# Kernel optimization log

Hardware: AMD Instinct MI355X
Metric: run time of the kernel (lower is better)

The kernel has to match this reference:

```python
import jax, jax.numpy as jnp
import numpy as np

M, K, N = 8192, 4096, 4096  # tokens, in_features, out_features
QMAX = 127.0


def setup_inputs() -> dict:
    key = jax.random.key(0)
    kx, kw, ks, kb = jax.random.split(key, 4)
    x = jax.random.normal(kx, (M, K), dtype=jnp.float32)
    # Build w_q / s_w the same way from_float would: per-output-channel symmetric quant
    w = jax.random.normal(kw, (N, K), dtype=jnp.float32) * 0.02
    s_w = (jnp.max(jnp.abs(w), axis=1, keepdims=True) / QMAX).astype(jnp.float32)  # [N,1]
    w_q = jnp.clip(jnp.round(w / s_w), -QMAX, QMAX).astype(jnp.int8)  # [N,K] int8
    bias = jax.random.normal(kb, (N,), dtype=jnp.float32) * 0.01
    return {"x": x, "w_q": w_q, "s_w": s_w, "bias": bias}


def reference(x, w_q, s_w, bias):
    # mode == 'W8A8_dynamic': per-tensor symmetric activation quant (zp = 0)
    s_x = jnp.max(jnp.abs(x)) / QMAX                       # scalar scale
    x_q = jnp.clip(jnp.round(x / s_x), -QMAX, QMAX)        # int8 values held in fp32
    # fake-dequant matmul: (x_q @ w_q^T) * (s_x * s_w^T) + bias
    y_int = x_q @ w_q.astype(jnp.float32).T                # [M, N]
    y = y_int * (s_x * s_w.astype(jnp.float32).T)          # broadcast [1,N]
    y = y + bias
    return y.astype(x.dtype)
```

## Files before the change

kernel.cpp:

```cpp
#include <hip/hip_runtime.h>
#include <stdint.h>

#define QMAXF 127.0f

constexpr int Mdim = 8192;
constexpr int Kdim = 4096;
constexpr int Ndim = 4096;
constexpr int PREP_BLOCKS = 2048;

using i32x4 = __attribute__((ext_vector_type(4))) int;

__device__ __forceinline__ void async_copy16(const void* g, void* l) {
    __builtin_amdgcn_global_load_lds(
        (const __attribute__((address_space(1))) void*)g,
        (__attribute__((address_space(3))) void*)l,
        16, 0, 0);
}

__global__ void prep_kernel(const float* __restrict__ x,
                            const int* __restrict__ w32,
                            float* __restrict__ blockmax,
                            int8_t* __restrict__ w8) {
    float m = 0.f;
    const float4* x4 = (const float4*)x;
    const int n4x = Mdim * Kdim / 4;
    for (int i = blockIdx.x * blockDim.x + threadIdx.x; i < n4x;
         i += gridDim.x * blockDim.x) {
        float4 v = x4[i];
        m = fmaxf(fmaxf(fabsf(v.x), fabsf(v.y)),
                  fmaxf(m, fmaxf(fabsf(v.z), fabsf(v.w))));
    }
#pragma unroll
    for (int off = 32; off > 0; off >>= 1)
        m = fmaxf(m, __shfl_down(m, off, 64));
    __shared__ float red[4];
    if ((threadIdx.x & 63) == 0) red[threadIdx.x >> 6] = m;
    __syncthreads();
    if (threadIdx.x == 0)
        blockmax[blockIdx.x] =
            fmaxf(fmaxf(red[0], red[1]), fmaxf(red[2], red[3]));

    const int4* in4 = (const int4*)w32;
    char4* out4 = (char4*)w8;
    const int n4w = Ndim * Kdim / 4;
    for (int i = blockIdx.x * blockDim.x + threadIdx.x; i < n4w;
         i += gridDim.x * blockDim.x) {
        int4 v = in4[i];
        char4 c;
        c.x = (signed char)v.x;
        c.y = (signed char)v.y;
        c.z = (signed char)v.z;
        c.w = (signed char)v.w;
        out4[i] = c;
    }
}

__global__ void finalize_kernel(const float* __restrict__ blockmax,
                                float* __restrict__ sx) {
    float m = 0.f;
    for (int i = threadIdx.x; i < PREP_BLOCKS; i += 256)
        m = fmaxf(m, blockmax[i]);
#pragma unroll
    for (int off = 32; off > 0; off >>= 1)
        m = fmaxf(m, __shfl_down(m, off, 64));
    __shared__ float red[4];
    if ((threadIdx.x & 63) == 0) red[threadIdx.x >> 6] = m;
    __syncthreads();
    if (threadIdx.x == 0)
        *sx = fmaxf(fmaxf(red[0], red[1]), fmaxf(red[2], red[3])) / QMAXF;
}

__global__ void quant_x_kernel(const float* __restrict__ x,
                               const float* __restrict__ sxp,
                               int8_t* __restrict__ xq, int n4) {
    const float s = *sxp;
    const float4* x4 = (const float4*)x;
    char4* q4 = (char4*)xq;
    for (int i = blockIdx.x * blockDim.x + threadIdx.x; i < n4;
         i += gridDim.x * blockDim.x) {
        float4 v = x4[i];
        char4 q;
        q.x = (signed char)(int)fminf(QMAXF, fmaxf(-QMAXF, rintf(v.x / s)));
        q.y = (signed char)(int)fminf(QMAXF, fmaxf(-QMAXF, rintf(v.y / s)));
        q.z = (signed char)(int)fminf(QMAXF, fmaxf(-QMAXF, rintf(v.z / s)));
        q.w = (signed char)(int)fminf(QMAXF, fmaxf(-QMAXF, rintf(v.w / s)));
        q4[i] = q;
    }
}

#define BM 256
#define BN 256
#define BKB 128
#define NKT (Kdim / BKB)

#define BAR() __builtin_amdgcn_s_barrier()
#define LGKM0()                                           \
    do {                                                  \
        asm volatile("s_waitcnt lgkmcnt(0)" ::: "memory");\
        __builtin_amdgcn_sched_barrier(0);                \
    } while (0)

__global__ __launch_bounds__(512, 2) void gemm_i8_kernel(
    const int8_t* __restrict__ Xq, const int8_t* __restrict__ Wq,
    const float* __restrict__ sxp, const float* __restrict__ s_w,
    const float* __restrict__ bias, float* __restrict__ Y) {
    __shared__ int8_t lds[131072];

    const int t = threadIdx.x;
    const int w = t >> 6;
    const int l = t & 63;
    const int lane15 = l & 15;
    const int lquad = l >> 4;
    const int swz7 = l & 7;

    const int flat = blockIdx.y * gridDim.x + blockIdx.x;
    const int swzb = (flat & 7) * 64 + (flat >> 3);
    const int bn = (swzb & 15) * BN;
    const int bm = (swzb >> 4) * BM;

    const int r0 = t >> 3;
    const int cOff = ((t & 7) ^ (r0 & 7)) * 16;
    const int8_t* aS = Xq + (size_t)(bm + r0) * Kdim + cOff;
    const int8_t* bS = Wq + (size_t)(bn + r0) * Kdim + cOff;
    const int wb = w * 1024;

    const int aRdBase = ((w >> 2) * 64 + lane15) * BKB;
    const int bRdBase = ((w & 3) * 32 + lane15) * BKB;
    const int kOff0 = (lquad ^ swz7) * 16;
    const int kOff1 = kOff0 ^ 64;

    i32x4 acc[2][2][4][2] = {};
    i32x4 a[4][2], b[2][2];

    int8_t* const ldsA_ = lds;
    int8_t* const ldsB_ = lds + 32768;

#define STAGE(SRC, LBASE, h, kt)                                              \
    do {                                                                      \
        if ((kt) < NKT) {                                                     \
            const int8_t* _s =                                                \
                (SRC) + (size_t)(h) * 128 * Kdim + (size_t)(kt) * BKB;        \
            int8_t* _d = (LBASE) + ((kt) & 1) * 65536 + (h) * 16384 + wb;     \
            async_copy16(_s, _d);                                             \
            async_copy16(_s + (size_t)64 * Kdim, _d + 8192);                  \
        }                                                                     \
    } while (0)

#define LDA(mh)                                                               \
    {                                                                         \
        _Pragma("unroll") for (int i = 0; i < 4; ++i) {                       \
            a[i][0] = *(const i32x4*)(curA + aRdBase + (mh) * 16384 +         \
                                      i * 2048 + kOff0);                      \
            a[i][1] = *(const i32x4*)(curA + aRdBase + (mh) * 16384 +         \
                                      i * 2048 + kOff1);                      \
        }                                                                     \
    }

#define LDB(nh)                                                               \
    {                                                                         \
        _Pragma("unroll") for (int j = 0; j < 2; ++j) {                       \
            b[j][0] = *(const i32x4*)(curB + bRdBase + (nh) * 16384 +         \
                                      j * 2048 + kOff0);                      \
            b[j][1] = *(const i32x4*)(curB + bRdBase + (nh) * 16384 +         \
                                      j * 2048 + kOff1);                      \
        }                                                                     \
    }

#define MFMA_Q(mh, nh)                                                        \
    do {                                                                      \
        __builtin_amdgcn_s_setprio(1);                                        \
        _Pragma("unroll") for (int i = 0; i < 4; ++i)                         \
            _Pragma("unroll") for (int j = 0; j < 2; ++j) {                   \
            acc[mh][nh][i][j] = __builtin_amdgcn_mfma_i32_16x16x64_i8(        \
                a[i][0], b[j][0], acc[mh][nh][i][j], 0, 0, 0);                \
            acc[mh][nh][i][j] = __builtin_amdgcn_mfma_i32_16x16x64_i8(        \
                a[i][1], b[j][1], acc[mh][nh][i][j], 0, 0, 0);                \
        }                                                                     \
        __builtin_amdgcn_s_setprio(0);                                        \
    } while (0)

#define GROUP(T, BOFF)                                                        \
    do {                                                                      \
        const int8_t* curA = ldsA_ + (BOFF);                                  \
        const int8_t* curB = ldsB_ + (BOFF);                                  \
                                                                      \
        LDA(0); LDB(0);                                                       \
        STAGE(bS, ldsB_, 0, (T) + 1);                                         \
        asm volatile("s_waitcnt lgkmcnt(8)" ::: "memory");                    \
        BAR(); LGKM0(); MFMA_Q(0, 0); BAR();                                  \
                                                                      \
        LDB(1);                                                               \
        STAGE(aS, ldsA_, 0, (T) + 2);                                         \
        BAR(); LGKM0(); MFMA_Q(0, 1); BAR();                                  \
                                                                      \
        LDA(1);                                                               \
        STAGE(bS, ldsB_, 1, (T) + 2);                                         \
        BAR(); LGKM0(); MFMA_Q(1, 1); BAR();                                  \
                                                                      \
        LDB(0);                                                               \
        STAGE(aS, ldsA_, 1, (T) + 2);                                         \
        if ((T) + 2 < NKT) {                                                  \
            asm volatile("s_waitcnt vmcnt(6)" ::: "memory");                  \
        } else {                                                              \
            asm volatile("s_waitcnt vmcnt(0)" ::: "memory");                  \
        }                                                                     \
        BAR(); LGKM0(); MFMA_Q(1, 0); BAR();                                  \
    } while (0)

    STAGE(aS, ldsA_, 0, 0);
    STAGE(bS, ldsB_, 1, 0);
    STAGE(aS, ldsA_, 1, 0);
    STAGE(bS, ldsB_, 0, 0);
    STAGE(aS, ldsA_, 0, 1);
    STAGE(bS, ldsB_, 1, 1);
    STAGE(aS, ldsA_, 1, 1);
    asm volatile("s_waitcnt vmcnt(6)" ::: "memory");
    BAR();

    for (int t2 = 0; t2 < NKT; t2 += 2) {
        GROUP(t2, 0);
        GROUP(t2 + 1, 65536);
    }

    const float sx = *sxp;
    const int wmE = (w >> 2) * 64;
    const int wnE = (w & 3) * 32;
#pragma unroll
    for (int nh = 0; nh < 2; ++nh) {
#pragma unroll
        for (int j = 0; j < 2; ++j) {
            const int col = bn + nh * 128 + wnE + j * 16 + lane15;
            const float sc = sx * s_w[col];
            const float bs = bias[col];
#pragma unroll
            for (int mh = 0; mh < 2; ++mh) {
#pragma unroll
                for (int i = 0; i < 4; ++i) {
                    const int row = bm + mh * 128 + wmE + i * 16 + lquad * 4;
                    float* yp = Y + (size_t)row * Ndim + col;
#pragma unroll
                    for (int r = 0; r < 4; ++r)
                        yp[(size_t)r * Ndim] =
                            (float)acc[mh][nh][i][j][r] * sc + bs;
                }
            }
        }
    }
}

extern "C" void kernel_launch(void* const* d_in, const int* in_sizes, int n_in,
                              void* d_out, int out_size, void* d_ws,
                              size_t ws_size, hipStream_t stream) {
    const float* x = (const float*)d_in[0];
    const int* w_q = (const int*)d_in[1];
    const float* s_w = (const float*)d_in[2];
    const float* bias = (const float*)d_in[3];
    float* y = (float*)d_out;

    float* sx = (float*)d_ws;
    float* blockmax = (float*)((char*)d_ws + 256);
    int8_t* xq = (int8_t*)d_ws + 16384;
    int8_t* wq8 = (int8_t*)d_ws + 16384 + (size_t)Mdim * Kdim;

    prep_kernel<<<PREP_BLOCKS, 256, 0, stream>>>(x, w_q, blockmax, wq8);
    finalize_kernel<<<1, 256, 0, stream>>>(blockmax, sx);
    quant_x_kernel<<<PREP_BLOCKS, 256, 0, stream>>>(x, sx, xq,
                                                    Mdim * Kdim / 4);

    dim3 grid(Ndim / BN, Mdim / BM);
    gemm_i8_kernel<<<grid, 512, 0, stream>>>(xq, wq8, sx, s_w, bias, y);
}
```

Measured before the change: 411.5 us.

## Double-buffer MFMA register fragments and halve barriers in int8 GEMM main loop

Restructures the K-loop pipeline so the A/B fragment registers are double-buffered (a0/a1, b0/b1). LDS fragment reads for the next quadrant, and for the next k-tile, are issued before the current MFMA block runs. Each quarter-step now has one barrier with partial lgkmcnt waits, where before it had two barriers plus a full LGKM wait. Out-of-range stages are clamped to reload valid tiles instead of being branched around, which keeps vmcnt counting uniform. The aim is to hide LDS latency behind MFMAs and cut synchronisation stalls, at the cost of more VGPRs and some redundant tail global loads.

```diff
diff --git a/kernel.cpp b/kernel.cpp
--- a/kernel.cpp
+++ b/kernel.cpp
@@ -93,12 +93,19 @@
 #define BKB 128
 #define NKT (Kdim / BKB)
 
-#define BAR() __builtin_amdgcn_s_barrier()
-#define LGKM0()                                           \
-    do {                                                  \
-        asm volatile("s_waitcnt lgkmcnt(0)" ::: "memory");\
-        __builtin_amdgcn_sched_barrier(0);                \
-    } while (0)
+#define BARF()                              \
+    do {                                    \
+        __builtin_amdgcn_s_barrier();       \
+        __builtin_amdgcn_sched_barrier(0);  \
+    } while (0)
+
+#define WAITLGKM(N)                                                  \
+    do {                                                             \
+        asm volatile("s_waitcnt lgkmcnt(" #N ")" ::: "memory");      \
+        __builtin_amdgcn_sched_barrier(0);                           \
+    } while (0)
+
+#define WAITVM(N) asm volatile("s_waitcnt vmcnt(" #N ")" ::: "memory")
 
 __global__ __launch_bounds__(512, 2) void gemm_i8_kernel(
     const int8_t* __restrict__ Xq, const int8_t* __restrict__ Wq,
@@ -111,7 +118,7 @@
     const int l = t & 63;
     const int lane15 = l & 15;
     const int lquad = l >> 4;
-    const int swz7 = l & 7;
+    const int swz7 = lane15 & 7;
 
     const int flat = blockIdx.y * gridDim.x + blockIdx.x;
     const int swzb = (flat & 7) * 64 + (flat >> 3);
@@ -130,96 +137,97 @@
     const int kOff1 = kOff0 ^ 64;
 
     i32x4 acc[2][2][4][2] = {};
-    i32x4 a[4][2], b[2][2];
+    i32x4 a0[4][2], a1[4][2], b0[2][2], b1[2][2];
 
     int8_t* const ldsA_ = lds;
     int8_t* const ldsB_ = lds + 32768;
 
 #define STAGE(SRC, LBASE, h, kt)                                              \
     do {                                                                      \
-        if ((kt) < NKT) {                                                     \
-            const int8_t* _s =                                                \
-                (SRC) + (size_t)(h) * 128 * Kdim + (size_t)(kt) * BKB;        \
-            int8_t* _d = (LBASE) + ((kt) & 1) * 65536 + (h) * 16384 + wb;     \
-            async_copy16(_s, _d);                                             \
-            async_copy16(_s + (size_t)64 * Kdim, _d + 8192);                  \
+        const int _kt = (kt) < NKT ? (kt) : (NKT - 2 + ((kt) & 1));           \
+        const int8_t* _s =                                                    \
+            (SRC) + (size_t)(h) * 128 * Kdim + (size_t)_kt * BKB;             \
+        int8_t* _d = (LBASE) + (_kt & 1) * 65536 + (h) * 16384 + wb;          \
+        async_copy16(_s, _d);                                                 \
+        async_copy16(_s + (size_t)64 * Kdim, _d + 8192);                      \
+    } while (0)
+
+#define LDFRAG_A(dst, BOFF, mh)                                               \
+    do {                                                                      \
+        const int8_t* _p = lds + (BOFF) + aRdBase + (mh) * 16384;             \
+        _Pragma("unroll") for (int i = 0; i < 4; ++i) {                       \
+            dst[i][0] = *(const i32x4*)(_p + i * 2048 + kOff0);               \
+            dst[i][1] = *(const i32x4*)(_p + i * 2048 + kOff1);               \
         }                                                                     \
     } while (0)
 
-#define LDA(mh)                                                               \
-    {                                                                         \
-        _Pragma("unroll") for (int i = 0; i < 4; ++i) {                       \
-            a[i][0] = *(const i32x4*)(curA + aRdBase + (mh) * 16384 +         \
-                                      i * 2048 + kOff0);                      \
-            a[i][1] = *(const i32x4*)(curA + aRdBase + (mh) * 16384 +         \
-                                      i * 2048 + kOff1);                      \
+#define LDFRAG_B(dst, BOFF, nh)                                               \
+    do {                                                                      \
+        const int8_t* _p = lds + 32768 + (BOFF) + bRdBase + (nh) * 16384;     \
+        _Pragma("unroll") for (int j = 0; j < 2; ++j) {                       \
+            dst[j][0] = *(const i32x4*)(_p + j * 2048 + kOff0);               \
+            dst[j][1] = *(const i32x4*)(_p + j * 2048 + kOff1);               \
         }                                                                     \
-    }
-
-#define LDB(nh)                                                               \
-    {                                                                         \
-        _Pragma("unroll") for (int j = 0; j < 2; ++j) {                       \
-            b[j][0] = *(const i32x4*)(curB + bRdBase + (nh) * 16384 +         \
-                                      j * 2048 + kOff0);                      \
-            b[j][1] = *(const i32x4*)(curB + bRdBase + (nh) * 16384 +         \
-                                      j * 2048 + kOff1);                      \
-        }                                                                     \
-    }
-
-#define MFMA_Q(mh, nh)                                                        \
+    } while (0)
+
+#define MFMAQ(mh, nh, A, B)                                                   \
     do {                                                                      \
         __builtin_amdgcn_s_setprio(1);                                        \
         _Pragma("unroll") for (int i = 0; i < 4; ++i)                         \
             _Pragma("unroll") for (int j = 0; j < 2; ++j) {                   \
-            acc[mh][nh][i][j] = __builtin_amdgcn_mfma_i32_16x16x64_i8(        \
-                a[i][0], b[j][0], acc[mh][nh][i][j], 0, 0, 0);                \
-            acc[mh][nh][i][j] = __builtin_amdgcn_mfma_i32_16x16x64_i8(        \
-                a[i][1], b[j][1], acc[mh][nh][i][j], 0, 0, 0);                \
-        }                                                                     \
+                acc[mh][nh][i][j] = __builtin_amdgcn_mfma_i32_16x16x64_i8(    \
+                    (A)[i][0], (B)[j][0], acc[mh][nh][i][j], 0, 0, 0);        \
+                acc[mh][nh][i][j] = __builtin_amdgcn_mfma_i32_16x16x64_i8(    \
+                    (A)[i][1], (B)[j][1], acc[mh][nh][i][j], 0, 0, 0);        \
+            }                                                                 \
         __builtin_amdgcn_s_setprio(0);                                        \
     } while (0)
 
-#define GROUP(T, BOFF)                                                        \
-    do {                                                                      \
-        const int8_t* curA = ldsA_ + (BOFF);                                  \
-        const int8_t* curB = ldsB_ + (BOFF);                                  \
-                                                                      \
-        LDA(0); LDB(0);                                                       \
-        STAGE(bS, ldsB_, 0, (T) + 1);                                         \
-        asm volatile("s_waitcnt lgkmcnt(8)" ::: "memory");                    \
-        BAR(); LGKM0(); MFMA_Q(0, 0); BAR();                                  \
-                                                                      \
-        LDB(1);                                                               \
+#define GROUP(T, BOFF, OBOFF)                                                 \
+    do {                                                                      \
+                                                                 \
+        LDFRAG_B(b1, BOFF, 1);                                                \
+        WAITLGKM(4);                                                          \
+        MFMAQ(0, 0, a0, b0);                                                  \
+        STAGE(bS, ldsB_, 1, (T) + 1);                                         \
+        WAITVM(6);                                                            \
+        BARF();                                                               \
+                                                                 \
+        LDFRAG_A(a1, BOFF, 1);                                                \
+        WAITLGKM(8);                                                          \
+        MFMAQ(0, 1, a0, b1);                                                  \
+        STAGE(aS, ldsA_, 1, (T) + 1);                                         \
+        WAITVM(6);                                                            \
+        BARF();                                                               \
+                                                                 \
+        LDFRAG_A(a0, OBOFF, 0);                                               \
+        WAITLGKM(8);                                                          \
+        MFMAQ(1, 1, a1, b1);                                                  \
         STAGE(aS, ldsA_, 0, (T) + 2);                                         \
-        BAR(); LGKM0(); MFMA_Q(0, 1); BAR();                                  \
-                                                                      \
-        LDA(1);                                                               \
-        STAGE(bS, ldsB_, 1, (T) + 2);                                         \
-        BAR(); LGKM0(); MFMA_Q(1, 1); BAR();                                  \
-                                                                      \
-        LDB(0);                                                               \
-        STAGE(aS, ldsA_, 1, (T) + 2);                                         \
-        if ((T) + 2 < NKT) {                                                  \
-            asm volatile("s_waitcnt vmcnt(6)" ::: "memory");                  \
-        } else {                                                              \
-            asm volatile("s_waitcnt vmcnt(0)" ::: "memory");                  \
-        }                                                                     \
-        BAR(); LGKM0(); MFMA_Q(1, 0); BAR();                                  \
+        WAITVM(6);                                                            \
+        BARF();                                                               \
+                                                                 \
+        MFMAQ(1, 0, a1, b0);                                                  \
+        LDFRAG_B(b0, OBOFF, 0);                                               \
+        STAGE(bS, ldsB_, 0, (T) + 2);                                         \
+        WAITVM(6);                                                            \
+        BARF();                                                               \
     } while (0)
 
     STAGE(aS, ldsA_, 0, 0);
+    STAGE(bS, ldsB_, 0, 0);
     STAGE(bS, ldsB_, 1, 0);
     STAGE(aS, ldsA_, 1, 0);
-    STAGE(bS, ldsB_, 0, 0);
     STAGE(aS, ldsA_, 0, 1);
-    STAGE(bS, ldsB_, 1, 1);
-    STAGE(aS, ldsA_, 1, 1);
-    asm volatile("s_waitcnt vmcnt(6)" ::: "memory");
-    BAR();
+    STAGE(bS, ldsB_, 0, 1);
+    WAITVM(6);
+    BARF();
+    LDFRAG_A(a0, 0, 0);
+    LDFRAG_B(b0, 0, 0);
 
     for (int t2 = 0; t2 < NKT; t2 += 2) {
-        GROUP(t2, 0);
-        GROUP(t2 + 1, 65536);
+        GROUP(t2, 0, 65536);
+        GROUP(t2 + 1, 65536, 0);
     }
 
     const float sx = *sxp;
```

New measurement: 404.5 us. Within noise of the previous version (-1.7%).
